# Optimization experiments

Hardware: AMD Instinct MI355X
Metric: run time of the kernel (lower is better)

The kernel has to match this reference:

```python
import jax, jax.numpy as jnp
import numpy as np

B, L, P, D, RD, NT = 128, 128, 1024, 128, 128, 256
SCALE = 1.0 / float(np.sqrt(D))


def _gelu(x):
    return jax.nn.gelu(x, approximate=False)


def _ln(x, g, b):
    mu = jnp.mean(x, axis=-1, keepdims=True)
    v = jnp.mean((x - mu) ** 2, axis=-1, keepdims=True)
    return (x - mu) * jax.lax.rsqrt(v + 1e-5) * g + b


def _mlp2(x, w1, b1, w2, b2):
    return _gelu(x @ w1 + b1) @ w2 + b2


def _l2norm(x):
    return x / jnp.maximum(jnp.sqrt(jnp.sum(x * x, axis=-1, keepdims=True)), 1e-12)


def _params(key):
    ks = jax.random.split(key, 16)
    def lin(k, i, o):
        return jax.random.normal(k, (i, o), jnp.float32) * (1.0 / float(np.sqrt(i)))
    z = lambda *s: jnp.zeros(s, jnp.float32)
    o = lambda *s: jnp.ones(s, jnp.float32)
    p = {}
    p['lt_emb'] = jax.random.normal(ks[0], (NT, D), jnp.float32) * 0.02
    p['lx_w1'] = lin(ks[1], 8, D); p['lx_b1'] = z(D)
    p['lx_w2'] = lin(ks[2], D, D); p['lx_b2'] = z(D)
    p['l_ln_g'] = o(D); p['l_ln_b'] = z(D)
    p['pt_emb'] = jax.random.normal(ks[3], (NT, D), jnp.float32) * 0.02
    p['px_w1'] = lin(ks[4], 192, D); p['px_b1'] = z(D)
    p['px_w2'] = lin(ks[5], D, D); p['px_b2'] = z(D)
    p['ps_w1'] = lin(ks[6], 1, D); p['ps_b1'] = z(D)
    p['ps_w2'] = lin(ks[7], D, D); p['ps_b2'] = z(D)
    p['p_ln_g'] = o(D); p['p_ln_b'] = z(D)
    p['proj_l_w'] = lin(ks[8], D, D)
    p['proj_p_w'] = lin(ks[9], D, D)
    p['dustbin_vec'] = jax.random.normal(ks[10], (D,), jnp.float32) * 0.02
    p['sg_w1'] = lin(ks[11], D, D); p['sg_b1'] = z(D)
    p['sg_w2'] = lin(ks[12], D, 1); p['sg_b2'] = z(1)
    p['retr_l_w'] = lin(ks[13], D, RD)
    p['retr_p_w'] = lin(ks[14], D, RD)
    return p


def setup_inputs():
    key = jax.random.key(0)
    kd = jax.random.split(key, 10)
    inp = {
        'l_x': jax.random.normal(kd[0], (B, L, 8), jnp.float32),
        'l_typ': jax.random.randint(kd[1], (B, L), 0, NT),
        'p_x': jax.random.normal(kd[2], (B, P, 192), jnp.float32),
        'p_typ': jax.random.randint(kd[3], (B, P), 0, NT),
        'p_score': jax.random.normal(kd[4], (B, P), jnp.float32),
        'p_rad': jax.random.uniform(kd[5], (B, P), jnp.float32),
        'l_mask': jax.random.bernoulli(kd[6], 0.9, (B, L)).at[:, 0].set(True),
        'p_mask': jax.random.bernoulli(kd[7], 0.9, (B, P)).at[:, 0].set(True),
    }
    inp.update(_params(kd[8]))
    return inp


def reference(l_x, l_typ, p_x, p_typ, p_score, p_rad, l_mask, p_mask,
              lt_emb, lx_w1, lx_b1, lx_w2, lx_b2, l_ln_g, l_ln_b,
              pt_emb, px_w1, px_b1, px_w2, px_b2, ps_w1, ps_b1, ps_w2, ps_b2,
              p_ln_g, p_ln_b, proj_l_w, proj_p_w, dustbin_vec,
              sg_w1, sg_b1, sg_w2, sg_b2, retr_l_w, retr_p_w):
    # --- encode_batch ---
    hL = _ln(_mlp2(l_x, lx_w1, lx_b1, lx_w2, lx_b2)
             + lt_emb[jnp.clip(l_typ, 0, NT - 1)], l_ln_g, l_ln_b) @ proj_l_w
    hP = _ln(_mlp2(p_x, px_w1, px_b1, px_w2, px_b2)
             + pt_emb[jnp.clip(p_typ, 0, NT - 1)]
             + _mlp2(p_score[..., None], ps_w1, ps_b1, ps_w2, ps_b2), p_ln_g, p_ln_b) @ proj_p_w
    neg = jnp.finfo(jnp.float32).min
    # --- feature_logits_batch: masked bilinear similarity ---
    logits = jnp.einsum('bld,bpd->blp', hL, hP) * SCALE  # [B,L,P]
    logits = jnp.where(p_mask[:, None, :], logits, neg)
    logits = jnp.where(l_mask[:, :, None], logits, neg)
    # --- assignment_logW_batch with dustbin ---
    dust = (hL @ dustbin_vec) * SCALE  # [B,L]
    full = jnp.concatenate([logits, dust[:, :, None]], axis=-1)  # [B,L,P+1]
    full = jnp.where(l_mask[:, :, None], full, neg)
    logW = jax.nn.log_softmax(full, axis=-1)
    # --- invariant_feature_terms_batch ---
    W = jnp.exp(logW)
    lm = l_mask.astype(jnp.float32)
    pm = p_mask.astype(jnp.float32)
    denom = jnp.maximum(lm.sum(axis=1), 1.0)  # [B]
    Wm = jnp.concatenate([W[..., :-1] * pm[:, None, :], W[..., -1:]], axis=-1)
    sharp = (Wm.max(axis=-1) * lm).sum(axis=1) / denom
    ent = ((-(Wm * logW)).sum(axis=-1) * lm).sum(axis=1) / denom
    neg_ent = -ent
    # --- pooled_embeddings_batch ---
    l_g = (hL * lm[..., None]).sum(axis=1) / jnp.maximum(lm.sum(axis=1)[:, None], 1.0)
    p_g = (hP * pm[..., None]).sum(axis=1) / jnp.maximum(pm.sum(axis=1)[:, None], 1.0)
    l_z = _l2norm(l_g @ retr_l_w)
    p_z = _l2norm(p_g @ retr_p_w)
    # --- pocket_sigma_nodes_batch ---
    sig = jax.nn.softplus((_gelu(hP @ sg_w1 + sg_b1) @ sg_w2 + sg_b2)[..., 0]) + 1e-3 + jnp.maximum(p_rad, 0.0)
    return logW, sharp, neg_ent, l_z, p_z, sig
```

## Files before the change

kernel.cpp:

```cpp
#include <hip/hip_runtime.h>
#include <hip/hip_bf16.h>
#include <math.h>

#define B_ 128
#define L_ 128
#define P_ 1024
#define D_ 128
#define NT_ 256

#define NEGF (-__FLT_MAX__)
#define SCALE_ 0.08838834764831845f
#define CLAMPV 1e30f

#define OUT_SHARP  16793600
#define OUT_NEGENT 16793728
#define OUT_LZ     16793856
#define OUT_PZ     16810240
#define OUT_SIG    16826624

#define WS_HLB    0
#define WS_HPB    1048576
#define WS_DUST   9437184
#define WS_SHARPP 9453568
#define WS_ENTP   9454592
#define WS_FLAG   9455616
#define WS_WT     9455632
#define WS_PPART  9500696
#define WS_PCNT   10024984

using bh8  = __attribute__((ext_vector_type(8))) short;
using fx4  = __attribute__((ext_vector_type(4))) float;

__device__ __forceinline__ float gelu_(float x) {
    float c = x * x;
    float v = x * fmaf(c, 0.07135481584f, 1.5957691216f);
    return x * __builtin_amdgcn_rcpf(1.0f + __expf(-v));
}
__device__ __forceinline__ float bf2f(unsigned short u) {
    return __uint_as_float(((unsigned)u) << 16);
}
__device__ __forceinline__ float sanz(float x) {
    return fminf(fmaxf(x, -CLAMPV), CLAMPV);
}
template<int BF> __device__ __forceinline__ float ldf(const void* p, int i) {
    if constexpr (BF) return bf2f(((const unsigned short*)p)[i]);
    else return ((const float*)p)[i];
}
template<int BF> __device__ __forceinline__ void stf(void* p, size_t i, float x) {
    x = sanz(x);
    if constexpr (BF) ((__hip_bfloat16*)p)[i] = __float2bfloat16(x);
    else ((float*)p)[i] = x;
}
__device__ __forceinline__ float maskf(const void* m, int mm, int idx) {
    if (mm == 3) return ((const float*)m)[idx] != 0.f ? 1.f : 0.f;
    if (mm == 2) return ((const unsigned short*)m)[idx] ? 1.f : 0.f;
    if (mm == 1) return ((const unsigned char*)m)[idx] ? 1.f : 0.f;
    return ((const int*)m)[idx] ? 1.f : 0.f;
}
__device__ __forceinline__ int typf(const void* p, int tm, int idx) {
    int v;
    if (tm == 2) v = (int)bf2f(((const unsigned short*)p)[idx]);
    else if (tm == 1) v = (int)((const long long*)p)[idx];
    else v = ((const int*)p)[idx];
    return v < 0 ? 0 : (v > NT_ - 1 ? NT_ - 1 : v);
}

__global__ __launch_bounds__(64) void detect_k(const unsigned int* __restrict__ px,
                                               const unsigned int* __restrict__ pm,
                                               const unsigned int* __restrict__ pt,
                                               int* __restrict__ flags)
{
    const int t = threadIdx.x;
    int hit = 0;
    for (int i = t; i < 4096; i += 64) {
        unsigned e = (px[i] >> 7) & 0xFFu;
        hit += (e >= 110 && e <= 132) ? 1 : 0;
    }
    for (int s = 1; s < 64; s <<= 1) hit += __shfl_xor(hit, s);

    unsigned big = 0, lo3f = 0, hi3f = 0;
    for (int i = t; i < 1024; i += 64) {
        unsigned wv = pm[i];
        big  |= (wv > 1u) ? 1u : 0u;
        lo3f |= ((wv & 0xFFFFu) == 0x3F80u) ? 1u : 0u;
        hi3f |= ((wv >> 16) == 0x3F80u) ? 1u : 0u;
    }
    unsigned long long aBig = __ballot(big != 0), aLo = __ballot(lo3f != 0), aHi = __ballot(hi3f != 0);

    unsigned tbig = 0, oddnz = 0;
    for (int i = t; i < 512; i += 64) {
        unsigned we = pt[2 * i], wo = pt[2 * i + 1];
        tbig  |= (we > 0xFFFFu || wo > 0xFFFFu) ? 1u : 0u;
        oddnz |= (wo != 0u) ? 1u : 0u;
    }
    unsigned long long aTb = __ballot(tbig != 0), aOdd = __ballot(oddnz != 0);

    if (t == 0) {
        flags[1] = (hit > 2048) ? 1 : 0;
        flags[0] = aLo ? 2 : (aHi ? 3 : (aBig ? 1 : 0));
        flags[2] = aTb ? 2 : (!aOdd ? 1 : 0);
    }
}

template<int BF> __device__ __forceinline__ void wt_prep_body(
    const void* w1, const void* w2, const void* sw2,
    const void* proj, const void* gw1, __hip_bfloat16* wt)
{
    const int idx = blockIdx.x * 256 + threadIdx.x;
    const int stride = gridDim.x * 256;
    for (int i = idx; i < 128 * 192; i += stride) {
        int n = i / 192, k = i - n * 192;
        wt[n * 192 + k] = __float2bfloat16(ldf<BF>(w1, k * 128 + n));
    }
    __hip_bfloat16* w2c = wt + 24576;
    for (int i = idx; i < 128 * 256; i += stride) {
        int n = i >> 8, k = i & 255;
        float v = (k < 128) ? ldf<BF>(w2, k * 128 + n) : ldf<BF>(sw2, (k - 128) * 128 + n);
        w2c[n * 256 + k] = __float2bfloat16(v);
    }
    __hip_bfloat16* pjt = wt + 57344;
    for (int i = idx; i < 128 * 128; i += stride) {
        int n = i >> 7, k = i & 127;
        pjt[n * 128 + k] = __float2bfloat16(ldf<BF>(proj, k * 128 + n));
    }
    __hip_bfloat16* g1t = wt + 73728;
    for (int i = idx; i < 128 * 128; i += stride) {
        int n = i >> 7, k = i & 127;
        g1t[n * 128 + k] = __float2bfloat16(ldf<BF>(gw1, k * 128 + n));
    }
}

__global__ __launch_bounds__(256) void wt_prep_k(
    const void* w1, const void* w2, const void* sw2,
    const void* proj, const void* gw1, __hip_bfloat16* wt, const int* flags)
{
    if (flags[1]) wt_prep_body<1>(w1, w2, sw2, proj, gw1, wt);
    else          wt_prep_body<0>(w1, w2, sw2, proj, gw1, wt);
}

#define RL 8
template<int BF> __device__ __forceinline__ void enc_l_body(
    const void* l_x, const void* l_typ, int tm,
    const void* w1, const void* b1, const void* w2, const void* b2,
    const void* lng, const void* lnb, const void* emb, const void* proj,
    const void* dustv, __hip_bfloat16* hLb, float* dust)
{
    __shared__ __align__(16) float X[RL * 8];
    __shared__ __align__(16) float H[RL][D_];
    __shared__ __align__(16) float Y[RL][D_];
    __shared__ float mus[RL], rss[RL];
    const int o = threadIdx.x;
    const int base = blockIdx.x * RL;

    if (o < RL * 8) X[o] = ldf<BF>(l_x, base * 8 + o);
    __syncthreads();

    float acc[RL];
    const float b1o = ldf<BF>(b1, o);
#pragma unroll
    for (int r = 0; r < RL; r++) acc[r] = b1o;
#pragma unroll
    for (int i = 0; i < 8; i += 4) {
        float wa = ldf<BF>(w1, (i + 0) * D_ + o), wb = ldf<BF>(w1, (i + 1) * D_ + o);
        float wc = ldf<BF>(w1, (i + 2) * D_ + o), wd = ldf<BF>(w1, (i + 3) * D_ + o);
#pragma unroll
        for (int r = 0; r < RL; r++) {
            const float4 x4 = *(const float4*)&X[r * 8 + i];
            acc[r] = fmaf(x4.x, wa, fmaf(x4.y, wb, fmaf(x4.z, wc, fmaf(x4.w, wd, acc[r]))));
        }
    }
#pragma unroll
    for (int r = 0; r < RL; r++) H[r][o] = gelu_(acc[r]);
    __syncthreads();

#pragma unroll
    for (int r = 0; r < RL; r++) {
        int tt = typf(l_typ, tm, base + r);
        acc[r] = ldf<BF>(b2, o) + ldf<BF>(emb, tt * D_ + o);
    }
    for (int i = 0; i < D_; i += 4) {
        float wa = ldf<BF>(w2, (i + 0) * D_ + o), wb = ldf<BF>(w2, (i + 1) * D_ + o);
        float wc = ldf<BF>(w2, (i + 2) * D_ + o), wd = ldf<BF>(w2, (i + 3) * D_ + o);
#pragma unroll
        for (int r = 0; r < RL; r++) {
            const float4 h4 = *(const float4*)&H[r][i];
            acc[r] = fmaf(h4.x, wa, fmaf(h4.y, wb, fmaf(h4.z, wc, fmaf(h4.w, wd, acc[r]))));
        }
    }
#pragma unroll
    for (int r = 0; r < RL; r++) Y[r][o] = acc[r];
    __syncthreads();

    {
        const int r = o >> 4, j = o & 15;
        float s = 0.f;
#pragma unroll
        for (int i = 0; i < 8; i++) s += Y[r][j * 8 + i];
        s += __shfl_xor(s, 1); s += __shfl_xor(s, 2); s += __shfl_xor(s, 4); s += __shfl_xor(s, 8);
        const float mu = s * (1.f / 128.f);
        float v = 0.f;
#pragma unroll
        for (int i = 0; i < 8; i++) { float d = Y[r][j * 8 + i] - mu; v = fmaf(d, d, v); }
        v += __shfl_xor(v, 1); v += __shfl_xor(v, 2); v += __shfl_xor(v, 4); v += __shfl_xor(v, 8);
        if (j == 0) { mus[r] = mu; rss[r] = rsqrtf(v * (1.f / 128.f) + 1e-5f); }
    }
    __syncthreads();
    {
        const float g = ldf<BF>(lng, o), bl = ldf<BF>(lnb, o);
#pragma unroll
        for (int r = 0; r < RL; r++) Y[r][o] = fmaf((Y[r][o] - mus[r]) * rss[r], g, bl);
    }
    __syncthreads();

#pragma unroll
    for (int r = 0; r < RL; r++) acc[r] = 0.f;
    for (int i = 0; i < D_; i += 4) {
        float wa = ldf<BF>(proj, (i + 0) * D_ + o), wb = ldf<BF>(proj, (i + 1) * D_ + o);
        float wc = ldf<BF>(proj, (i + 2) * D_ + o), wd = ldf<BF>(proj, (i + 3) * D_ + o);
#pragma unroll
        for (int r = 0; r < RL; r++) {
            const float4 y4 = *(const float4*)&Y[r][i];
            acc[r] = fmaf(y4.x, wa, fmaf(y4.y, wb, fmaf(y4.z, wc, fmaf(y4.w, wd, acc[r]))));
        }
    }
    const float dvo = ldf<BF>(dustv, o);
#pragma unroll
    for (int r = 0; r < RL; r++) {
        hLb[(size_t)(base + r) * D_ + o] = __float2bfloat16(acc[r]);
        H[r][o] = acc[r] * dvo;
    }
    __syncthreads();
    {
        const int r = o >> 4, j = o & 15;
        float s = 0.f;
#pragma unroll
        for (int i = 0; i < 8; i++) s += H[r][j * 8 + i];
        s += __shfl_xor(s, 1); s += __shfl_xor(s, 2); s += __shfl_xor(s, 4); s += __shfl_xor(s, 8);
        if (j == 0) dust[base + r] = s * SCALE_;
    }
}

__global__ __launch_bounds__(128) void enc_l_k(
    const void* l_x, const void* l_typ,
    const void* w1, const void* b1, const void* w2, const void* b2,
    const void* lng, const void* lnb, const void* emb, const void* proj,
    const void* dustv, __hip_bfloat16* hLb, float* dust, const int* flags)
{
    const int tm = flags[2];
    if (flags[1]) enc_l_body<1>(l_x, l_typ, tm, w1, b1, w2, b2, lng, lnb, emb, proj, dustv, hLb, dust);
    else          enc_l_body<0>(l_x, l_typ, tm, w1, b1, w2, b2, lng, lnb, emb, proj, dustv, hLb, dust);
}

#define XS 264
#define ROWS 64
#define ENC_P_SMEM 36608
template<int BF> __device__ __forceinline__ void enc_p_body(
    unsigned short* X, float* red1, float* red2, float* pm_s, float* sc_s, int* tt_s,
    const void* p_x, const void* p_typ, int tm,
    const void* p_score, const void* p_rad,
    const void* b1, const void* b2, const void* sb2,
    const void* sw1, const void* sb1,
    const void* lng, const void* lnb, const void* emb,
    const void* gb1, const void* gw2, const void* gb2,
    const unsigned short* wt, const void* p_mask, int mm,
    void* out, __hip_bfloat16* hPb, float* ppart, float* pcnt)
{
    const int t = threadIdx.x;
    const int o = t & 127, rh = t >> 7;
    const int lane = t & 63, w = t >> 6;
    const int m = lane & 15, g = lane >> 4;
    const int b = blockIdx.x >> 4, tile = blockIdx.x & 15;
    const int base = b * P_ + tile * ROWS;
    const int c0 = 32 * w + m, c1 = 32 * w + 16 + m;
    __hip_bfloat16* Xb = (__hip_bfloat16*)X;

    if constexpr (BF) {
        const unsigned short* src = (const unsigned short*)p_x + (size_t)base * 192;
#pragma unroll
        for (int i = t * 8; i < ROWS * 192; i += 256 * 8) {
            const int r = i / 192, k = i - r * 192;
            *(bh8*)(X + r * XS + k) = *(const bh8*)(src + i);
        }
    } else {
        for (int i = t; i < ROWS * 192; i += 256) {
            int r = i / 192, k = i - r * 192;
            Xb[r * XS + k] = __float2bfloat16(((const float*)p_x)[(size_t)base * 192 + i]);
        }
    }
    if (t < ROWS) {
        pm_s[t] = maskf(p_mask, mm, base + t);
        sc_s[t] = ldf<BF>(p_score, base + t);
        tt_s[t] = typf(p_typ, tm, base + t);
    }
    __syncthreads();

    fx4 A1[4][2];
#pragma unroll
    for (int mt = 0; mt < 4; mt++) { A1[mt][0] = fx4{0,0,0,0}; A1[mt][1] = fx4{0,0,0,0}; }
    {
        const unsigned short* q0 = wt + ((2 * w + 0) * 16 + m) * 192 + g * 8;
        const unsigned short* q1 = wt + ((2 * w + 1) * 16 + m) * 192 + g * 8;
#pragma unroll
        for (int ks = 0; ks < 6; ks++) {
            bh8 f0 = *(const bh8*)(q0 + ks * 32);
            bh8 f1 = *(const bh8*)(q1 + ks * 32);
#pragma unroll
            for (int mt = 0; mt < 4; mt++) {
                bh8 a = *(const bh8*)(X + (mt * 16 + m) * XS + g * 8 + ks * 32);
                A1[mt][0] = __builtin_amdgcn_mfma_f32_16x16x32_bf16(a, f0, A1[mt][0], 0, 0, 0);
                A1[mt][1] = __builtin_amdgcn_mfma_f32_16x16x32_bf16(a, f1, A1[mt][1], 0, 0, 0);
            }
        }
    }
    __syncthreads();

    {
        const float bb0 = ldf<BF>(b1, c0), bb1 = ldf<BF>(b1, c1);
#pragma unroll
        for (int mt = 0; mt < 4; mt++)
#pragma unroll
            for (int j = 0; j < 4; j++) {
                const int row = mt * 16 + g * 4 + j;
                Xb[row * XS + c0] = __float2bfloat16(gelu_(A1[mt][0][j] + bb0));
                Xb[row * XS + c1] = __float2bfloat16(gelu_(A1[mt][1][j] + bb1));
            }
    }
    {
        const float a1v = ldf<BF>(sw1, o), a0v = ldf<BF>(sb1, o);
#pragma unroll
        for (int r = 0; r < 32; r++) {
            const int row = rh * 32 + r;
            Xb[row * XS + 128 + o] = __float2bfloat16(gelu_(fmaf(sc_s[row], a1v, a0v)));
        }
    }
    __syncthreads();

    fx4 A2[4][2];
#pragma unroll
    for (int mt = 0; mt < 4; mt++) { A2[mt][0] = fx4{0,0,0,0}; A2[mt][1] = fx4{0,0,0,0}; }
    {
        const unsigned short* w2cT = wt + 24576;
        const unsigned short* q0 = w2cT + ((2 * w + 0) * 16 + m) * 256 + g * 8;
        const unsigned short* q1 = w2cT + ((2 * w + 1) * 16 + m) * 256 + g * 8;
#pragma unroll
        for (int ks = 0; ks < 8; ks++) {
            bh8 f0 = *(const bh8*)(q0 + ks * 32);
            bh8 f1 = *(const bh8*)(q1 + ks * 32);
#pragma unroll
            for (int mt = 0; mt < 4; mt++) {
                bh8 a = *(const bh8*)(X + (mt * 16 + m) * XS + g * 8 + ks * 32);
                A2[mt][0] = __builtin_amdgcn_mfma_f32_16x16x32_bf16(a, f0, A2[mt][0], 0, 0, 0);
                A2[mt][1] = __builtin_amdgcn_mfma_f32_16x16x32_bf16(a, f1, A2[mt][1], 0, 0, 0);
            }
        }
    }
    {
        const float bc0 = ldf<BF>(b2, c0) + ldf<BF>(sb2, c0);
        const float bc1 = ldf<BF>(b2, c1) + ldf<BF>(sb2, c1);
#pragma unroll
        for (int mt = 0; mt < 4; mt++)
#pragma unroll
            for (int j = 0; j < 4; j++) {
                const int row = mt * 16 + g * 4 + j;
                const int tt = tt_s[row];
                A2[mt][0][j] += bc0 + ldf<BF>(emb, tt * D_ + c0);
                A2[mt][1][j] += bc1 + ldf<BF>(emb, tt * D_ + c1);
            }
    }
#pragma unroll
    for (int mt = 0; mt < 4; mt++)
#pragma unroll
        for (int j = 0; j < 4; j++) {
            const int row = mt * 16 + g * 4 + j;
            float s = A2[mt][0][j] + A2[mt][1][j];
            float q = fmaf(A2[mt][0][j], A2[mt][0][j], A2[mt][1][j] * A2[mt][1][j]);
            s += __shfl_xor(s, 1); s += __shfl_xor(s, 2); s += __shfl_xor(s, 4); s += __shfl_xor(s, 8);
            q += __shfl_xor(q, 1); q += __shfl_xor(q, 2); q += __shfl_xor(q, 4); q += __shfl_xor(q, 8);
            if (m == 0) { red1[row * 4 + w] = s; red2[row * 4 + w] = q; }
        }
    __syncthreads();
    {
        const float gc0 = ldf<BF>(lng, c0), bl0 = ldf<BF>(lnb, c0);
        const float gc1 = ldf<BF>(lng, c1), bl1 = ldf<BF>(lnb, c1);
#pragma unroll
        for (int mt = 0; mt < 4; mt++)
#pragma unroll
            for (int j = 0; j < 4; j++) {
                const int row = mt * 16 + g * 4 + j;
                float S = (red1[row * 4 + 0] + red1[row * 4 + 1]) + (red1[row * 4 + 2] + red1[row * 4 + 3]);
                float Q = (red2[row * 4 + 0] + red2[row * 4 + 1]) + (red2[row * 4 + 2] + red2[row * 4 + 3]);
                float mu = S * (1.f / 128.f);
                float var = fmaf(Q, 1.f / 128.f, -mu * mu);
                float rs = rsqrtf(var + 1e-5f);
                float y0 = fmaf((A2[mt][0][j] - mu) * rs, gc0, bl0);
                float y1 = fmaf((A2[mt][1][j] - mu) * rs, gc1, bl1);
                Xb[row * XS + c0] = __float2bfloat16(y0);
                Xb[row * XS + c1] = __float2bfloat16(y1);
            }
    }
    __syncthreads();

    fx4 A3[4][2];
#pragma unroll
    for (int mt = 0; mt < 4; mt++) { A3[mt][0] = fx4{0,0,0,0}; A3[mt][1] = fx4{0,0,0,0}; }
    {
        const unsigned short* pjT = wt + 57344;
        const unsigned short* q0 = pjT + ((2 * w + 0) * 16 + m) * 128 + g * 8;
        const unsigned short* q1 = pjT + ((2 * w + 1) * 16 + m) * 128 + g * 8;
#pragma unroll
        for (int ks = 0; ks < 4; ks++) {
            bh8 f0 = *(const bh8*)(q0 + ks * 32);
            bh8 f1 = *(const bh8*)(q1 + ks * 32);
#pragma unroll
            for (int mt = 0; mt < 4; mt++) {
                bh8 a = *(const bh8*)(X + (mt * 16 + m) * XS + g * 8 + ks * 32);
                A3[mt][0] = __builtin_amdgcn_mfma_f32_16x16x32_bf16(a, f0, A3[mt][0], 0, 0, 0);
                A3[mt][1] = __builtin_amdgcn_mfma_f32_16x16x32_bf16(a, f1, A3[mt][1], 0, 0, 0);
            }
        }
    }
    __syncthreads();

    {
#pragma unroll
        for (int mt = 0; mt < 4; mt++)
#pragma unroll
            for (int j = 0; j < 4; j++) {
                const int row = mt * 16 + g * 4 + j;
                __hip_bfloat16 h0 = __float2bfloat16(A3[mt][0][j]);
                __hip_bfloat16 h1 = __float2bfloat16(A3[mt][1][j]);
                hPb[(size_t)(base + row) * D_ + c0] = h0;
                hPb[(size_t)(base + row) * D_ + c1] = h1;
                Xb[row * XS + c0] = h0;
                Xb[row * XS + c1] = h1;
            }
        float ps0 = 0.f, ps1 = 0.f;
#pragma unroll
        for (int mt = 0; mt < 4; mt++)
#pragma unroll
            for (int j = 0; j < 4; j++) {
                const int row = mt * 16 + g * 4 + j;
                ps0 = fmaf(A3[mt][0][j], pm_s[row], ps0);
                ps1 = fmaf(A3[mt][1][j], pm_s[row], ps1);
            }
        ps0 += __shfl_xor(ps0, 16); ps0 += __shfl_xor(ps0, 32);
        ps1 += __shfl_xor(ps1, 16); ps1 += __shfl_xor(ps1, 32);
        if (g == 0) {
            ppart[(size_t)blockIdx.x * D_ + c0] = ps0;
            ppart[(size_t)blockIdx.x * D_ + c1] = ps1;
        }
        if (t == 0) {
            float c = 0.f;
#pragma unroll
            for (int r = 0; r < ROWS; r++) c += pm_s[r];
            pcnt[blockIdx.x] = c;
        }
    }
    __syncthreads();

    fx4 A4[4][2];
#pragma unroll
    for (int mt = 0; mt < 4; mt++) { A4[mt][0] = fx4{0,0,0,0}; A4[mt][1] = fx4{0,0,0,0}; }
    {
        const unsigned short* g1T = wt + 73728;
        const unsigned short* q0 = g1T + ((2 * w + 0) * 16 + m) * 128 + g * 8;
        const unsigned short* q1 = g1T + ((2 * w + 1) * 16 + m) * 128 + g * 8;
#pragma unroll
        for (int ks = 0; ks < 4; ks++) {
            bh8 f0 = *(const bh8*)(q0 + ks * 32);
            bh8 f1 = *(const bh8*)(q1 + ks * 32);
#pragma unroll
            for (int mt = 0; mt < 4; mt++) {
                bh8 a = *(const bh8*)(X + (mt * 16 + m) * XS + g * 8 + ks * 32);
                A4[mt][0] = __builtin_amdgcn_mfma_f32_16x16x32_bf16(a, f0, A4[mt][0], 0, 0, 0);
                A4[mt][1] = __builtin_amdgcn_mfma_f32_16x16x32_bf16(a, f1, A4[mt][1], 0, 0, 0);
            }
        }
    }
    {
        const float gb0 = ldf<BF>(gb1, c0), gb1v = ldf<BF>(gb1, c1);
        const float w20 = ldf<BF>(gw2, c0), w21 = ldf<BF>(gw2, c1);
#pragma unroll
        for (int mt = 0; mt < 4; mt++)
#pragma unroll
            for (int j = 0; j < 4; j++) {
                const int row = mt * 16 + g * 4 + j;
                float g0 = gelu_(A4[mt][0][j] + gb0);
                float g1v = gelu_(A4[mt][1][j] + gb1v);
                float p = fmaf(g0, w20, g1v * w21);
                p += __shfl_xor(p, 1); p += __shfl_xor(p, 2); p += __shfl_xor(p, 4); p += __shfl_xor(p, 8);
                if (m == 0) red1[row * 4 + w] = p;
            }
    }
    __syncthreads();
    if (t < ROWS) {
        float s = (red1[t * 4 + 0] + red1[t * 4 + 1]) + (red1[t * 4 + 2] + red1[t * 4 + 3]);
        float v = s + ldf<BF>(gb2, 0);
        float sp = fmaxf(v, 0.f) + log1pf(expf(-fabsf(v)));
        stf<BF>(out, (size_t)OUT_SIG + base + t, sp + 1e-3f + fmaxf(ldf<BF>(p_rad, base + t), 0.f));
    }
}

__global__ __launch_bounds__(256) void enc_p_k(
    const void* p_x, const void* p_typ, const void* p_score, const void* p_rad,
    const void* b1, const void* b2, const void* sb2,
    const void* sw1, const void* sb1,
    const void* lng, const void* lnb, const void* emb,
    const void* gb1, const void* gw2, const void* gb2,
    const unsigned short* wt, const void* p_mask, const int* flags,
    void* out, __hip_bfloat16* hPb, float* ppart, float* pcnt)
{
    extern __shared__ __align__(16) char smem[];
    unsigned short* X = (unsigned short*)smem;
    float* red1 = (float*)(smem + 33792);
    float* red2 = (float*)(smem + 34816);
    float* pm_s = (float*)(smem + 35840);
    float* sc_s = (float*)(smem + 36096);
    int*   tt_s = (int*)(smem + 36352);
    const int tm = flags[2], mm = flags[0];
    if (flags[1]) enc_p_body<1>(X, red1, red2, pm_s, sc_s, tt_s,
                                p_x, p_typ, tm, p_score, p_rad, b1, b2, sb2, sw1, sb1,
                                lng, lnb, emb, gb1, gw2, gb2, wt, p_mask, mm,
                                out, hPb, ppart, pcnt);
    else          enc_p_body<0>(X, red1, red2, pm_s, sc_s, tt_s,
                                p_x, p_typ, tm, p_score, p_rad, b1, b2, sb2, sw1, sb1,
                                lng, lnb, emb, gb1, gw2, gb2, wt, p_mask, mm,
                                out, hPb, ppart, pcnt);
}

template<int BF> __device__ __forceinline__ void logits_sm_body(
    const unsigned short* hLb, const unsigned short* hPb, const float* dust,
    const void* l_mask, const void* p_mask, int mm,
    void* out, float* sharp_parts, float* ent_parts)
{
    __shared__ float pm_s[1024];
    __shared__ float lm_s[16], dv_s[16];
    __shared__ float redA[64], redB[64], redC[64], redD[64], redM[16], redL[16];
    const int t = threadIdx.x;
    const int lane = t & 63, w = t >> 6;
    const int m = lane & 15, g = lane >> 4;
    const int b = blockIdx.x & 127, l0 = (blockIdx.x >> 7) * 16;

    for (int i = t; i < 1024; i += 256) pm_s[i] = maskf(p_mask, mm, b * P_ + i);
    if (t < 16) {
        lm_s[t] = maskf(l_mask, mm, b * L_ + l0 + t);
        dv_s[t] = dust[b * L_ + l0 + t];
    }
    __syncthreads();

    bh8 af[4];
    {
        const unsigned short* ha = hLb + ((size_t)(b * L_ + l0 + m)) * D_ + g * 8;
#pragma unroll
        for (int ks = 0; ks < 4; ks++) af[ks] = *(const bh8*)(ha + ks * 32);
    }
    const unsigned short* hpb = hPb + ((size_t)(b * P_ + w * 256)) * D_;

    fx4 acc[16];
#pragma unroll
    for (int nt = 0; nt < 16; nt++) {
        fx4 c = {0.f, 0.f, 0.f, 0.f};
        const unsigned short* hr = hpb + (nt * 16 + m) * D_ + g * 8;
#pragma unroll
        for (int ks = 0; ks < 4; ks++) {
            bh8 bfr = *(const bh8*)(hr + ks * 32);
            c = __builtin_amdgcn_mfma_f32_16x16x32_bf16(af[ks], bfr, c, 0, 0, 0);
        }
        acc[nt] = c;
    }

    float rmax[4] = {NEGF, NEGF, NEGF, NEGF};
#pragma unroll
    for (int nt = 0; nt < 16; nt++) {
        const float pv = pm_s[w * 256 + nt * 16 + m];
#pragma unroll
        for (int j = 0; j < 4; j++) {
            const bool ok = (lm_s[g * 4 + j] != 0.f) && (pv != 0.f);
            float v = ok ? acc[nt][j] * SCALE_ : NEGF;
            acc[nt][j] = v;
            rmax[j] = fmaxf(rmax[j], v);
        }
    }
#pragma unroll
    for (int j = 0; j < 4; j++) {
        rmax[j] = fmaxf(rmax[j], __shfl_xor(rmax[j], 1));
        rmax[j] = fmaxf(rmax[j], __shfl_xor(rmax[j], 2));
// ... 52 lines not shown
            float lwc = fmaxf(lw, -CLAMPV);
            float wm = __expf(lwc) * pv;
            mw[j] = fmaxf(mw[j], wm);
            if (wm > 0.f) es[j] = fmaf(-wm, lwc, es[j]);
        }
    }
#pragma unroll
    for (int j = 0; j < 4; j++) {
        mw[j] = fmaxf(mw[j], __shfl_xor(mw[j], 1));
        mw[j] = fmaxf(mw[j], __shfl_xor(mw[j], 2));
        mw[j] = fmaxf(mw[j], __shfl_xor(mw[j], 4));
        mw[j] = fmaxf(mw[j], __shfl_xor(mw[j], 8));
        es[j] += __shfl_xor(es[j], 1); es[j] += __shfl_xor(es[j], 2);
        es[j] += __shfl_xor(es[j], 4); es[j] += __shfl_xor(es[j], 8);
    }
    if (m == 0) {
#pragma unroll
        for (int j = 0; j < 4; j++) {
            redC[(g * 4 + j) * 4 + w] = mw[j];
            redD[(g * 4 + j) * 4 + w] = es[j];
        }
    }
    __syncthreads();
    if (t < 16) {
        float dvr = (lm_s[t] != 0.f) ? dv_s[t] : NEGF;
        stf<BF>(out, (size_t)(b * L_ + l0 + t) * (P_ + 1) + P_, dvr - redM[t] - redL[t]);
    }
    if (t == 0) {
        float sp = 0.f, en = 0.f;
        for (int r = 0; r < 16; r++) {
            float dvr = (lm_s[r] != 0.f) ? dv_s[r] : NEGF;
            float lwd = fmaxf(dvr - redM[r] - redL[r], -CLAMPV);
            float wd = __expf(lwd);
            float mwr = fmaxf(fmaxf(redC[r * 4 + 0], redC[r * 4 + 1]), fmaxf(redC[r * 4 + 2], redC[r * 4 + 3]));
            mwr = fmaxf(mwr, wd);
            float esr = (redD[r * 4 + 0] + redD[r * 4 + 1]) + (redD[r * 4 + 2] + redD[r * 4 + 3]);
            if (wd > 0.f) esr = fmaf(-wd, lwd, esr);
            sp = fmaf(mwr, lm_s[r], sp);
            en = fmaf(esr, lm_s[r], en);
        }
        sharp_parts[blockIdx.x] = sp;
        ent_parts[blockIdx.x] = en;
    }
}

__global__ __launch_bounds__(256) void logits_sm_k(
    const unsigned short* hLb, const unsigned short* hPb, const float* dust,
    const void* l_mask, const void* p_mask, const int* flags,
    void* out, float* sharp_parts, float* ent_parts)
{
    const int mm = flags[0];
    if (flags[1]) logits_sm_body<1>(hLb, hPb, dust, l_mask, p_mask, mm, out, sharp_parts, ent_parts);
    else          logits_sm_body<0>(hLb, hPb, dust, l_mask, p_mask, mm, out, sharp_parts, ent_parts);
}

template<int BF> __device__ __forceinline__ void epilogue_body(
    const unsigned short* hLb, const void* l_mask, int mm,
    const void* retr_l, const void* retr_p,
    const float* ppart, const float* pcnt,
    const float* sharp_parts, const float* ent_parts, void* out)
{
    __shared__ float lmv[L_];
    __shared__ __align__(16) float lg[D_];
    __shared__ __align__(16) float pgs[D_];
    __shared__ float red[4];
    const int o = threadIdx.x, b = blockIdx.x;
    lmv[o] = maskf(l_mask, mm, b * L_ + o);
    __syncthreads();
    float cnt = 0.f;
    for (int l = 0; l < L_; l++) cnt += lmv[l];
    {
        float s0 = 0, s1 = 0, s2 = 0, s3 = 0;
        const unsigned short* hb = hLb + (size_t)b * L_ * D_;
        for (int l = 0; l < L_; l += 4) {
            s0 = fmaf(bf2f(hb[(l + 0) * D_ + o]), lmv[l + 0], s0);
            s1 = fmaf(bf2f(hb[(l + 1) * D_ + o]), lmv[l + 1], s1);
            s2 = fmaf(bf2f(hb[(l + 2) * D_ + o]), lmv[l + 2], s2);
            s3 = fmaf(bf2f(hb[(l + 3) * D_ + o]), lmv[l + 3], s3);
        }
        lg[o] = ((s0 + s1) + (s2 + s3)) / fmaxf(cnt, 1.f);
    }
    {
        float s = 0.f, c = 0.f;
        for (int k = 0; k < 16; k++) s += ppart[(size_t)(b * 16 + k) * D_ + o];
        for (int k = 0; k < 16; k++) c += pcnt[b * 16 + k];
        pgs[o] = s / fmaxf(c, 1.f);
    }
    __syncthreads();
    float rL = 0.f, rP = 0.f;
    for (int i = 0; i < D_; i += 4) {
        const float4 g4 = *(const float4*)&lg[i];
        rL = fmaf(g4.x, ldf<BF>(retr_l, (i + 0) * D_ + o), rL);
        rL = fmaf(g4.y, ldf<BF>(retr_l, (i + 1) * D_ + o), rL);
        rL = fmaf(g4.z, ldf<BF>(retr_l, (i + 2) * D_ + o), rL);
        rL = fmaf(g4.w, ldf<BF>(retr_l, (i + 3) * D_ + o), rL);
        const float4 p4 = *(const float4*)&pgs[i];
        rP = fmaf(p4.x, ldf<BF>(retr_p, (i + 0) * D_ + o), rP);
        rP = fmaf(p4.y, ldf<BF>(retr_p, (i + 1) * D_ + o), rP);
        rP = fmaf(p4.z, ldf<BF>(retr_p, (i + 2) * D_ + o), rP);
        rP = fmaf(p4.w, ldf<BF>(retr_p, (i + 3) * D_ + o), rP);
    }
    float nL = rL * rL, nP = rP * rP;
    nL += __shfl_xor(nL, 1); nL += __shfl_xor(nL, 2); nL += __shfl_xor(nL, 4);
    nL += __shfl_xor(nL, 8); nL += __shfl_xor(nL, 16); nL += __shfl_xor(nL, 32);
    nP += __shfl_xor(nP, 1); nP += __shfl_xor(nP, 2); nP += __shfl_xor(nP, 4);
    nP += __shfl_xor(nP, 8); nP += __shfl_xor(nP, 16); nP += __shfl_xor(nP, 32);
    if ((o & 63) == 0) { red[o >> 6] = nL; red[2 + (o >> 6)] = nP; }
    __syncthreads();
    {
        float nrmL = fmaxf(sqrtf(red[0] + red[1]), 1e-12f);
        float nrmP = fmaxf(sqrtf(red[2] + red[3]), 1e-12f);
        stf<BF>(out, (size_t)OUT_LZ + b * D_ + o, rL / nrmL);
        stf<BF>(out, (size_t)OUT_PZ + b * D_ + o, rP / nrmP);
    }
    if (o == 0) {
        const float den = fmaxf(cnt, 1.f);
        float sp = 0.f, en = 0.f;
        for (int k = 0; k < 8; k++) { sp += sharp_parts[k * 128 + b]; en += ent_parts[k * 128 + b]; }
        stf<BF>(out, (size_t)OUT_SHARP + b, sp / den);
        stf<BF>(out, (size_t)OUT_NEGENT + b, -(en / den));
    }
}

__global__ __launch_bounds__(128) void epilogue_k(
    const unsigned short* hLb, const void* l_mask, const int* flags,
    const void* retr_l, const void* retr_p,
    const float* ppart, const float* pcnt,
    const float* sharp_parts, const float* ent_parts, void* out)
{
    const int mm = flags[0];
    if (flags[1]) epilogue_body<1>(hLb, l_mask, mm, retr_l, retr_p, ppart, pcnt, sharp_parts, ent_parts, out);
    else          epilogue_body<0>(hLb, l_mask, mm, retr_l, retr_p, ppart, pcnt, sharp_parts, ent_parts, out);
}

extern "C" void kernel_launch(void* const* d_in, const int* in_sizes, int n_in,
                              void* d_out, int out_size, void* d_ws, size_t ws_size,
                              hipStream_t stream)
{
    const void* l_x     = d_in[0];
    const void* l_typ   = d_in[1];
    const void* p_x     = d_in[2];
    const void* p_typ   = d_in[3];
    const void* p_score = d_in[4];
    const void* p_rad   = d_in[5];
    const void* l_mask  = d_in[6];
    const void* p_mask  = d_in[7];
    const void* lt_emb  = d_in[8];
    const void* lx_w1   = d_in[9];
    const void* lx_b1   = d_in[10];
    const void* lx_w2   = d_in[11];
    const void* lx_b2   = d_in[12];
    const void* l_ln_g  = d_in[13];
    const void* l_ln_b  = d_in[14];
    const void* pt_emb  = d_in[15];
    const void* px_w1   = d_in[16];
    const void* px_b1   = d_in[17];
    const void* px_w2   = d_in[18];
    const void* px_b2   = d_in[19];
    const void* ps_w1   = d_in[20];
    const void* ps_b1   = d_in[21];
    const void* ps_w2   = d_in[22];
    const void* ps_b2   = d_in[23];
    const void* p_ln_g  = d_in[24];
    const void* p_ln_b  = d_in[25];
    const void* proj_l  = d_in[26];
    const void* proj_p  = d_in[27];
    const void* dustv   = d_in[28];
    const void* sg_w1   = d_in[29];
    const void* sg_b1   = d_in[30];
    const void* sg_w2   = d_in[31];
    const void* sg_b2   = d_in[32];
    const void* retr_l  = d_in[33];
    const void* retr_p  = d_in[34];

    float* ws     = (float*)d_ws;
    __hip_bfloat16* hLb = (__hip_bfloat16*)(ws + WS_HLB);
    __hip_bfloat16* hPb = (__hip_bfloat16*)(ws + WS_HPB);
    float* dust   = ws + WS_DUST;
    float* sharpp = ws + WS_SHARPP;
    float* entp   = ws + WS_ENTP;
    int*   flags  = (int*)(ws + WS_FLAG);
    __hip_bfloat16* wt = (__hip_bfloat16*)(ws + WS_WT);
    float* ppart  = ws + WS_PPART;
    float* pcnt   = ws + WS_PCNT;

    detect_k<<<1, 64, 0, stream>>>((const unsigned int*)p_x, (const unsigned int*)p_mask,
                                   (const unsigned int*)p_typ, flags);
    wt_prep_k<<<64, 256, 0, stream>>>(px_w1, px_w2, ps_w2, proj_p, sg_w1, wt, flags);
    enc_l_k<<<(B_ * L_) / RL, 128, 0, stream>>>(l_x, l_typ, lx_w1, lx_b1, lx_w2, lx_b2,
                                                l_ln_g, l_ln_b, lt_emb, proj_l, dustv,
                                                hLb, dust, flags);
    enc_p_k<<<B_ * (P_ / ROWS), 256, ENC_P_SMEM, stream>>>(
        p_x, p_typ, p_score, p_rad,
        px_b1, px_b2, ps_b2, ps_w1, ps_b1,
        p_ln_g, p_ln_b, pt_emb,
        sg_b1, sg_w2, sg_b2,
        (const unsigned short*)wt, p_mask, flags,
        d_out, hPb, ppart, pcnt);
    logits_sm_k<<<B_ * 8, 256, 0, stream>>>((const unsigned short*)hLb, (const unsigned short*)hPb,
                                            dust, l_mask, p_mask, flags, d_out, sharpp, entp);
    epilogue_k<<<B_, 128, 0, stream>>>((const unsigned short*)hLb, l_mask, flags,
                                       retr_l, retr_p, ppart, pcnt, sharpp, entp, d_out);
}
```

Baseline: 204.0 us.

## Precompose proj_p and sg_w1 weights so both GEMMs share one pass

A new small kernel multiplies proj_p by sg_w1 once to form a fused weight, so the sigma head reads the post-LN activations directly instead of hP. This lets the encoder run the projection and the sigma first-layer GEMMs in a single MFMA loop over the same A fragments. It removes two block barriers and the write-back of hP into shared memory. The cost is higher register pressure from doubled accumulators, one extra launch, and slightly different numerics because hP is no longer rounded to bf16 before the second matmul.

```diff
diff --git a/kernel.cpp b/kernel.cpp
--- a/kernel.cpp
+++ b/kernel.cpp
@@ -104,7 +104,7 @@
 
 template<int BF> __device__ __forceinline__ void wt_prep_body(
     const void* w1, const void* w2, const void* sw2,
-    const void* proj, const void* gw1, __hip_bfloat16* wt)
+    const void* proj, __hip_bfloat16* wt)
 {
     const int idx = blockIdx.x * 256 + threadIdx.x;
     const int stride = gridDim.x * 256;
@@ -123,19 +123,39 @@
         int n = i >> 7, k = i & 127;
         pjt[n * 128 + k] = __float2bfloat16(ldf<BF>(proj, k * 128 + n));
     }
-    __hip_bfloat16* g1t = wt + 73728;
-    for (int i = idx; i < 128 * 128; i += stride) {
-        int n = i >> 7, k = i & 127;
-        g1t[n * 128 + k] = __float2bfloat16(ldf<BF>(gw1, k * 128 + n));
-    }
 }
 
 __global__ __launch_bounds__(256) void wt_prep_k(
     const void* w1, const void* w2, const void* sw2,
-    const void* proj, const void* gw1, __hip_bfloat16* wt, const int* flags)
-{
-    if (flags[1]) wt_prep_body<1>(w1, w2, sw2, proj, gw1, wt);
-    else          wt_prep_body<0>(w1, w2, sw2, proj, gw1, wt);
+    const void* proj, __hip_bfloat16* wt, const int* flags)
+{
+    if (flags[1]) wt_prep_body<1>(w1, w2, sw2, proj, wt);
+    else          wt_prep_body<0>(w1, w2, sw2, proj, wt);
+}
+
+__global__ __launch_bounds__(256) void fuse_k(const void* proj, const void* gw1,
+                                              __hip_bfloat16* pg1, const int* flags)
+{
+    const int BF = flags[1];
+    const int tid = blockIdx.x * 256 + threadIdx.x;
+    const int e = tid >> 2, ll = tid & 3;
+    const int n = e >> 7, k = e & 127;
+    float s = 0.f;
+    if (BF) {
+        const unsigned short* pj = (const unsigned short*)proj + k * 128 + ll * 32;
+        const unsigned short* g1 = (const unsigned short*)gw1;
+#pragma unroll 8
+        for (int d = 0; d < 32; d++)
+            s = fmaf(bf2f(pj[d]), bf2f(g1[(ll * 32 + d) * 128 + n]), s);
+    } else {
+        const float* pj = (const float*)proj + k * 128 + ll * 32;
+        const float* g1 = (const float*)gw1;
+#pragma unroll 8
+        for (int d = 0; d < 32; d++)
+            s = fmaf(pj[d], g1[(ll * 32 + d) * 128 + n], s);
+    }
+    s += __shfl_xor(s, 1); s += __shfl_xor(s, 2);
+    if (ll == 0) pg1[n * 128 + k] = __float2bfloat16(s);
 }
 
 #define RL 8
@@ -400,26 +420,35 @@
     }
     __syncthreads();
 
-    fx4 A3[4][2];
-#pragma unroll
-    for (int mt = 0; mt < 4; mt++) { A3[mt][0] = fx4{0,0,0,0}; A3[mt][1] = fx4{0,0,0,0}; }
+    fx4 A3[4][2], A4[4][2];
+#pragma unroll
+    for (int mt = 0; mt < 4; mt++) {
+        A3[mt][0] = fx4{0,0,0,0}; A3[mt][1] = fx4{0,0,0,0};
+        A4[mt][0] = fx4{0,0,0,0}; A4[mt][1] = fx4{0,0,0,0};
+    }
     {
         const unsigned short* pjT = wt + 57344;
-        const unsigned short* q0 = pjT + ((2 * w + 0) * 16 + m) * 128 + g * 8;
-        const unsigned short* q1 = pjT + ((2 * w + 1) * 16 + m) * 128 + g * 8;
+        const unsigned short* pg1 = wt + 73728;
+        const unsigned short* q30 = pjT + ((2 * w + 0) * 16 + m) * 128 + g * 8;
+        const unsigned short* q31 = pjT + ((2 * w + 1) * 16 + m) * 128 + g * 8;
+        const unsigned short* q40 = pg1 + ((2 * w + 0) * 16 + m) * 128 + g * 8;
+        const unsigned short* q41 = pg1 + ((2 * w + 1) * 16 + m) * 128 + g * 8;
 #pragma unroll
         for (int ks = 0; ks < 4; ks++) {
-            bh8 f0 = *(const bh8*)(q0 + ks * 32);
-            bh8 f1 = *(const bh8*)(q1 + ks * 32);
+            bh8 f30 = *(const bh8*)(q30 + ks * 32);
+            bh8 f31 = *(const bh8*)(q31 + ks * 32);
+            bh8 f40 = *(const bh8*)(q40 + ks * 32);
+            bh8 f41 = *(const bh8*)(q41 + ks * 32);
 #pragma unroll
             for (int mt = 0; mt < 4; mt++) {
                 bh8 a = *(const bh8*)(X + (mt * 16 + m) * XS + g * 8 + ks * 32);
-                A3[mt][0] = __builtin_amdgcn_mfma_f32_16x16x32_bf16(a, f0, A3[mt][0], 0, 0, 0);
-                A3[mt][1] = __builtin_amdgcn_mfma_f32_16x16x32_bf16(a, f1, A3[mt][1], 0, 0, 0);
+                A3[mt][0] = __builtin_amdgcn_mfma_f32_16x16x32_bf16(a, f30, A3[mt][0], 0, 0, 0);
+                A3[mt][1] = __builtin_amdgcn_mfma_f32_16x16x32_bf16(a, f31, A3[mt][1], 0, 0, 0);
+                A4[mt][0] = __builtin_amdgcn_mfma_f32_16x16x32_bf16(a, f40, A4[mt][0], 0, 0, 0);
+                A4[mt][1] = __builtin_amdgcn_mfma_f32_16x16x32_bf16(a, f41, A4[mt][1], 0, 0, 0);
             }
         }
     }
-    __syncthreads();
 
     {
 #pragma unroll
@@ -427,12 +456,8 @@
 #pragma unroll
             for (int j = 0; j < 4; j++) {
                 const int row = mt * 16 + g * 4 + j;
-                __hip_bfloat16 h0 = __float2bfloat16(A3[mt][0][j]);
-                __hip_bfloat16 h1 = __float2bfloat16(A3[mt][1][j]);
-                hPb[(size_t)(base + row) * D_ + c0] = h0;
-                hPb[(size_t)(base + row) * D_ + c1] = h1;
-                Xb[row * XS + c0] = h0;
-                Xb[row * XS + c1] = h1;
+                hPb[(size_t)(base + row) * D_ + c0] = __float2bfloat16(A3[mt][0][j]);
+                hPb[(size_t)(base + row) * D_ + c1] = __float2bfloat16(A3[mt][1][j]);
             }
         float ps0 = 0.f, ps1 = 0.f;
 #pragma unroll
@@ -456,27 +481,7 @@
             pcnt[blockIdx.x] = c;
         }
     }
-    __syncthreads();
-
-    fx4 A4[4][2];
-#pragma unroll
-    for (int mt = 0; mt < 4; mt++) { A4[mt][0] = fx4{0,0,0,0}; A4[mt][1] = fx4{0,0,0,0}; }
-    {
-        const unsigned short* g1T = wt + 73728;
-        const unsigned short* q0 = g1T + ((2 * w + 0) * 16 + m) * 128 + g * 8;
-        const unsigned short* q1 = g1T + ((2 * w + 1) * 16 + m) * 128 + g * 8;
-#pragma unroll
-        for (int ks = 0; ks < 4; ks++) {
-            bh8 f0 = *(const bh8*)(q0 + ks * 32);
-            bh8 f1 = *(const bh8*)(q1 + ks * 32);
-#pragma unroll
-            for (int mt = 0; mt < 4; mt++) {
-                bh8 a = *(const bh8*)(X + (mt * 16 + m) * XS + g * 8 + ks * 32);
-                A4[mt][0] = __builtin_amdgcn_mfma_f32_16x16x32_bf16(a, f0, A4[mt][0], 0, 0, 0);
-                A4[mt][1] = __builtin_amdgcn_mfma_f32_16x16x32_bf16(a, f1, A4[mt][1], 0, 0, 0);
-            }
-        }
-    }
+
     {
         const float gb0 = ldf<BF>(gb1, c0), gb1v = ldf<BF>(gb1, c1);
         const float w20 = ldf<BF>(gw2, c0), w21 = ldf<BF>(gw2, c1);
@@ -824,7 +829,8 @@
 
     detect_k<<<1, 64, 0, stream>>>((const unsigned int*)p_x, (const unsigned int*)p_mask,
                                    (const unsigned int*)p_typ, flags);
-    wt_prep_k<<<64, 256, 0, stream>>>(px_w1, px_w2, ps_w2, proj_p, sg_w1, wt, flags);
+    wt_prep_k<<<64, 256, 0, stream>>>(px_w1, px_w2, ps_w2, proj_p, wt, flags);
+    fuse_k<<<256, 256, 0, stream>>>(proj_p, sg_w1, wt + 73728, flags);
     enc_l_k<<<(B_ * L_) / RL, 128, 0, stream>>>(l_x, l_typ, lx_w1, lx_b1, lx_w2, lx_b2,
                                                 l_ln_g, l_ln_b, lt_emb, proj_l, dustv,
                                                 hLb, dust, flags);
```

New measurement: 220.0 us. +7.9%, slower.

## Split pocket encoder tile across 8 waves with 2x4 M/N wave grid

Applied to the files above, without the earlier changes.

The pocket encoder block grows from 256 to 512 threads. Waves are arranged as 2 row groups by 4 column groups, so each wave computes 32 rows instead of 64 in every MFMA stage. Per-thread accumulator registers are halved and each block gets more waves to hide LDS and MFMA latency. In exchange, each wave group writes its own pooled partial sum, so the epilogue reduces 32 partials per batch, and the ppart workspace must hold twice as many entries.

```diff
diff --git a/kernel.cpp b/kernel.cpp
--- a/kernel.cpp
+++ b/kernel.cpp
@@ -268,21 +268,23 @@
     const int t = threadIdx.x;
     const int o = t & 127, rh = t >> 7;
     const int lane = t & 63, w = t >> 6;
+    const int wn = w & 3, wm = w >> 2;
     const int m = lane & 15, g = lane >> 4;
     const int b = blockIdx.x >> 4, tile = blockIdx.x & 15;
     const int base = b * P_ + tile * ROWS;
-    const int c0 = 32 * w + m, c1 = 32 * w + 16 + m;
+    const int c0 = 32 * wn + m, c1 = 32 * wn + 16 + m;
+    const int mtb = 2 * wm;
     __hip_bfloat16* Xb = (__hip_bfloat16*)X;
 
     if constexpr (BF) {
         const unsigned short* src = (const unsigned short*)p_x + (size_t)base * 192;
 #pragma unroll
-        for (int i = t * 8; i < ROWS * 192; i += 256 * 8) {
+        for (int i = t * 8; i < ROWS * 192; i += 512 * 8) {
             const int r = i / 192, k = i - r * 192;
             *(bh8*)(X + r * XS + k) = *(const bh8*)(src + i);
         }
     } else {
-        for (int i = t; i < ROWS * 192; i += 256) {
+        for (int i = t; i < ROWS * 192; i += 512) {
             int r = i / 192, k = i - r * 192;
             Xb[r * XS + k] = __float2bfloat16(((const float*)p_x)[(size_t)base * 192 + i]);
         }
@@ -294,19 +296,19 @@
     }
     __syncthreads();
 
-    fx4 A1[4][2];
-#pragma unroll
-    for (int mt = 0; mt < 4; mt++) { A1[mt][0] = fx4{0,0,0,0}; A1[mt][1] = fx4{0,0,0,0}; }
-    {
-        const unsigned short* q0 = wt + ((2 * w + 0) * 16 + m) * 192 + g * 8;
-        const unsigned short* q1 = wt + ((2 * w + 1) * 16 + m) * 192 + g * 8;
+    fx4 A1[2][2];
+#pragma unroll
+    for (int mt = 0; mt < 2; mt++) { A1[mt][0] = fx4{0,0,0,0}; A1[mt][1] = fx4{0,0,0,0}; }
+    {
+        const unsigned short* q0 = wt + ((2 * wn + 0) * 16 + m) * 192 + g * 8;
+        const unsigned short* q1 = wt + ((2 * wn + 1) * 16 + m) * 192 + g * 8;
 #pragma unroll
         for (int ks = 0; ks < 6; ks++) {
             bh8 f0 = *(const bh8*)(q0 + ks * 32);
             bh8 f1 = *(const bh8*)(q1 + ks * 32);
 #pragma unroll
-            for (int mt = 0; mt < 4; mt++) {
-                bh8 a = *(const bh8*)(X + (mt * 16 + m) * XS + g * 8 + ks * 32);
+            for (int mt = 0; mt < 2; mt++) {
+                bh8 a = *(const bh8*)(X + ((mtb + mt) * 16 + m) * XS + g * 8 + ks * 32);
                 A1[mt][0] = __builtin_amdgcn_mfma_f32_16x16x32_bf16(a, f0, A1[mt][0], 0, 0, 0);
                 A1[mt][1] = __builtin_amdgcn_mfma_f32_16x16x32_bf16(a, f1, A1[mt][1], 0, 0, 0);
             }
@@ -317,10 +319,10 @@
     {
         const float bb0 = ldf<BF>(b1, c0), bb1 = ldf<BF>(b1, c1);
 #pragma unroll
-        for (int mt = 0; mt < 4; mt++)
+        for (int mt = 0; mt < 2; mt++)
 #pragma unroll
             for (int j = 0; j < 4; j++) {
-                const int row = mt * 16 + g * 4 + j;
+                const int row = (mtb + mt) * 16 + g * 4 + j;
                 Xb[row * XS + c0] = __float2bfloat16(gelu_(A1[mt][0][j] + bb0));
                 Xb[row * XS + c1] = __float2bfloat16(gelu_(A1[mt][1][j] + bb1));
             }
@@ -328,27 +330,27 @@
     {
         const float a1v = ldf<BF>(sw1, o), a0v = ldf<BF>(sb1, o);
 #pragma unroll
-        for (int r = 0; r < 32; r++) {
-            const int row = rh * 32 + r;
+        for (int r = 0; r < 16; r++) {
+            const int row = rh * 16 + r;
             Xb[row * XS + 128 + o] = __float2bfloat16(gelu_(fmaf(sc_s[row], a1v, a0v)));
         }
     }
     __syncthreads();
 
-    fx4 A2[4][2];
-#pragma unroll
-    for (int mt = 0; mt < 4; mt++) { A2[mt][0] = fx4{0,0,0,0}; A2[mt][1] = fx4{0,0,0,0}; }
+    fx4 A2[2][2];
+#pragma unroll
+    for (int mt = 0; mt < 2; mt++) { A2[mt][0] = fx4{0,0,0,0}; A2[mt][1] = fx4{0,0,0,0}; }
     {
         const unsigned short* w2cT = wt + 24576;
-        const unsigned short* q0 = w2cT + ((2 * w + 0) * 16 + m) * 256 + g * 8;
-        const unsigned short* q1 = w2cT + ((2 * w + 1) * 16 + m) * 256 + g * 8;
+        const unsigned short* q0 = w2cT + ((2 * wn + 0) * 16 + m) * 256 + g * 8;
+        const unsigned short* q1 = w2cT + ((2 * wn + 1) * 16 + m) * 256 + g * 8;
 #pragma unroll
         for (int ks = 0; ks < 8; ks++) {
             bh8 f0 = *(const bh8*)(q0 + ks * 32);
             bh8 f1 = *(const bh8*)(q1 + ks * 32);
 #pragma unroll
-            for (int mt = 0; mt < 4; mt++) {
-                bh8 a = *(const bh8*)(X + (mt * 16 + m) * XS + g * 8 + ks * 32);
+            for (int mt = 0; mt < 2; mt++) {
+                bh8 a = *(const bh8*)(X + ((mtb + mt) * 16 + m) * XS + g * 8 + ks * 32);
                 A2[mt][0] = __builtin_amdgcn_mfma_f32_16x16x32_bf16(a, f0, A2[mt][0], 0, 0, 0);
                 A2[mt][1] = __builtin_amdgcn_mfma_f32_16x16x32_bf16(a, f1, A2[mt][1], 0, 0, 0);
             }
@@ -358,35 +360,35 @@
         const float bc0 = ldf<BF>(b2, c0) + ldf<BF>(sb2, c0);
         const float bc1 = ldf<BF>(b2, c1) + ldf<BF>(sb2, c1);
 #pragma unroll
-        for (int mt = 0; mt < 4; mt++)
+        for (int mt = 0; mt < 2; mt++)
 #pragma unroll
             for (int j = 0; j < 4; j++) {
-                const int row = mt * 16 + g * 4 + j;
+                const int row = (mtb + mt) * 16 + g * 4 + j;
                 const int tt = tt_s[row];
                 A2[mt][0][j] += bc0 + ldf<BF>(emb, tt * D_ + c0);
                 A2[mt][1][j] += bc1 + ldf<BF>(emb, tt * D_ + c1);
             }
     }
 #pragma unroll
-    for (int mt = 0; mt < 4; mt++)
+    for (int mt = 0; mt < 2; mt++)
 #pragma unroll
         for (int j = 0; j < 4; j++) {
-            const int row = mt * 16 + g * 4 + j;
+            const int row = (mtb + mt) * 16 + g * 4 + j;
             float s = A2[mt][0][j] + A2[mt][1][j];
             float q = fmaf(A2[mt][0][j], A2[mt][0][j], A2[mt][1][j] * A2[mt][1][j]);
             s += __shfl_xor(s, 1); s += __shfl_xor(s, 2); s += __shfl_xor(s, 4); s += __shfl_xor(s, 8);
             q += __shfl_xor(q, 1); q += __shfl_xor(q, 2); q += __shfl_xor(q, 4); q += __shfl_xor(q, 8);
-            if (m == 0) { red1[row * 4 + w] = s; red2[row * 4 + w] = q; }
+            if (m == 0) { red1[row * 4 + wn] = s; red2[row * 4 + wn] = q; }
         }
     __syncthreads();
     {
         const float gc0 = ldf<BF>(lng, c0), bl0 = ldf<BF>(lnb, c0);
         const float gc1 = ldf<BF>(lng, c1), bl1 = ldf<BF>(lnb, c1);
 #pragma unroll
-        for (int mt = 0; mt < 4; mt++)
+        for (int mt = 0; mt < 2; mt++)
 #pragma unroll
             for (int j = 0; j < 4; j++) {
-                const int row = mt * 16 + g * 4 + j;
+                const int row = (mtb + mt) * 16 + g * 4 + j;
                 float S = (red1[row * 4 + 0] + red1[row * 4 + 1]) + (red1[row * 4 + 2] + red1[row * 4 + 3]);
                 float Q = (red2[row * 4 + 0] + red2[row * 4 + 1]) + (red2[row * 4 + 2] + red2[row * 4 + 3]);
                 float mu = S * (1.f / 128.f);
@@ -400,20 +402,20 @@
     }
     __syncthreads();
 
-    fx4 A3[4][2];
-#pragma unroll
-    for (int mt = 0; mt < 4; mt++) { A3[mt][0] = fx4{0,0,0,0}; A3[mt][1] = fx4{0,0,0,0}; }
+    fx4 A3[2][2];
+#pragma unroll
+    for (int mt = 0; mt < 2; mt++) { A3[mt][0] = fx4{0,0,0,0}; A3[mt][1] = fx4{0,0,0,0}; }
     {
         const unsigned short* pjT = wt + 57344;
-        const unsigned short* q0 = pjT + ((2 * w + 0) * 16 + m) * 128 + g * 8;
-        const unsigned short* q1 = pjT + ((2 * w + 1) * 16 + m) * 128 + g * 8;
+        const unsigned short* q0 = pjT + ((2 * wn + 0) * 16 + m) * 128 + g * 8;
+        const unsigned short* q1 = pjT + ((2 * wn + 1) * 16 + m) * 128 + g * 8;
 #pragma unroll
         for (int ks = 0; ks < 4; ks++) {
             bh8 f0 = *(const bh8*)(q0 + ks * 32);
             bh8 f1 = *(const bh8*)(q1 + ks * 32);
 #pragma unroll
-            for (int mt = 0; mt < 4; mt++) {
-                bh8 a = *(const bh8*)(X + (mt * 16 + m) * XS + g * 8 + ks * 32);
+            for (int mt = 0; mt < 2; mt++) {
+                bh8 a = *(const bh8*)(X + ((mtb + mt) * 16 + m) * XS + g * 8 + ks * 32);
                 A3[mt][0] = __builtin_amdgcn_mfma_f32_16x16x32_bf16(a, f0, A3[mt][0], 0, 0, 0);
                 A3[mt][1] = __builtin_amdgcn_mfma_f32_16x16x32_bf16(a, f1, A3[mt][1], 0, 0, 0);
             }
@@ -423,10 +425,10 @@
 
     {
 #pragma unroll
-        for (int mt = 0; mt < 4; mt++)
+        for (int mt = 0; mt < 2; mt++)
 #pragma unroll
             for (int j = 0; j < 4; j++) {
-                const int row = mt * 16 + g * 4 + j;
+                const int row = (mtb + mt) * 16 + g * 4 + j;
                 __hip_bfloat16 h0 = __float2bfloat16(A3[mt][0][j]);
                 __hip_bfloat16 h1 = __float2bfloat16(A3[mt][1][j]);
                 hPb[(size_t)(base + row) * D_ + c0] = h0;
@@ -436,18 +438,18 @@
             }
         float ps0 = 0.f, ps1 = 0.f;
 #pragma unroll
-        for (int mt = 0; mt < 4; mt++)
+        for (int mt = 0; mt < 2; mt++)
 #pragma unroll
             for (int j = 0; j < 4; j++) {
-                const int row = mt * 16 + g * 4 + j;
+                const int row = (mtb + mt) * 16 + g * 4 + j;
                 ps0 = fmaf(A3[mt][0][j], pm_s[row], ps0);
                 ps1 = fmaf(A3[mt][1][j], pm_s[row], ps1);
             }
         ps0 += __shfl_xor(ps0, 16); ps0 += __shfl_xor(ps0, 32);
         ps1 += __shfl_xor(ps1, 16); ps1 += __shfl_xor(ps1, 32);
         if (g == 0) {
-            ppart[(size_t)blockIdx.x * D_ + c0] = ps0;
-            ppart[(size_t)blockIdx.x * D_ + c1] = ps1;
+            ppart[(size_t)(blockIdx.x * 2 + wm) * D_ + c0] = ps0;
+            ppart[(size_t)(blockIdx.x * 2 + wm) * D_ + c1] = ps1;
         }
         if (t == 0) {
             float c = 0.f;
@@ -458,20 +460,20 @@
     }
     __syncthreads();
 
-    fx4 A4[4][2];
-#pragma unroll
-    for (int mt = 0; mt < 4; mt++) { A4[mt][0] = fx4{0,0,0,0}; A4[mt][1] = fx4{0,0,0,0}; }
+    fx4 A4[2][2];
+#pragma unroll
+    for (int mt = 0; mt < 2; mt++) { A4[mt][0] = fx4{0,0,0,0}; A4[mt][1] = fx4{0,0,0,0}; }
     {
         const unsigned short* g1T = wt + 73728;
-        const unsigned short* q0 = g1T + ((2 * w + 0) * 16 + m) * 128 + g * 8;
-        const unsigned short* q1 = g1T + ((2 * w + 1) * 16 + m) * 128 + g * 8;
+        const unsigned short* q0 = g1T + ((2 * wn + 0) * 16 + m) * 128 + g * 8;
+        const unsigned short* q1 = g1T + ((2 * wn + 1) * 16 + m) * 128 + g * 8;
 #pragma unroll
         for (int ks = 0; ks < 4; ks++) {
             bh8 f0 = *(const bh8*)(q0 + ks * 32);
             bh8 f1 = *(const bh8*)(q1 + ks * 32);
 #pragma unroll
-            for (int mt = 0; mt < 4; mt++) {
-                bh8 a = *(const bh8*)(X + (mt * 16 + m) * XS + g * 8 + ks * 32);
+            for (int mt = 0; mt < 2; mt++) {
+                bh8 a = *(const bh8*)(X + ((mtb + mt) * 16 + m) * XS + g * 8 + ks * 32);
                 A4[mt][0] = __builtin_amdgcn_mfma_f32_16x16x32_bf16(a, f0, A4[mt][0], 0, 0, 0);
                 A4[mt][1] = __builtin_amdgcn_mfma_f32_16x16x32_bf16(a, f1, A4[mt][1], 0, 0, 0);
             }
@@ -481,15 +483,15 @@
         const float gb0 = ldf<BF>(gb1, c0), gb1v = ldf<BF>(gb1, c1);
         const float w20 = ldf<BF>(gw2, c0), w21 = ldf<BF>(gw2, c1);
 #pragma unroll
-        for (int mt = 0; mt < 4; mt++)
+        for (int mt = 0; mt < 2; mt++)
 #pragma unroll
             for (int j = 0; j < 4; j++) {
-                const int row = mt * 16 + g * 4 + j;
+                const int row = (mtb + mt) * 16 + g * 4 + j;
                 float g0 = gelu_(A4[mt][0][j] + gb0);
                 float g1v = gelu_(A4[mt][1][j] + gb1v);
                 float p = fmaf(g0, w20, g1v * w21);
                 p += __shfl_xor(p, 1); p += __shfl_xor(p, 2); p += __shfl_xor(p, 4); p += __shfl_xor(p, 8);
-                if (m == 0) red1[row * 4 + w] = p;
+                if (m == 0) red1[row * 4 + wn] = p;
             }
     }
     __syncthreads();
@@ -501,7 +503,7 @@
     }
 }
 
-__global__ __launch_bounds__(256) void enc_p_k(
+__global__ __launch_bounds__(512) void enc_p_k(
     const void* p_x, const void* p_typ, const void* p_score, const void* p_rad,
     const void* b1, const void* b2, const void* sb2,
     const void* sw1, const void* sb1,
@@ -720,7 +722,7 @@
     }
     {
         float s = 0.f, c = 0.f;
-        for (int k = 0; k < 16; k++) s += ppart[(size_t)(b * 16 + k) * D_ + o];
+        for (int k = 0; k < 32; k++) s += ppart[(size_t)(b * 32 + k) * D_ + o];
         for (int k = 0; k < 16; k++) c += pcnt[b * 16 + k];
         pgs[o] = s / fmaxf(c, 1.f);
     }
@@ -828,7 +830,7 @@
     enc_l_k<<<(B_ * L_) / RL, 128, 0, stream>>>(l_x, l_typ, lx_w1, lx_b1, lx_w2, lx_b2,
                                                 l_ln_g, l_ln_b, lt_emb, proj_l, dustv,
                                                 hLb, dust, flags);
-    enc_p_k<<<B_ * (P_ / ROWS), 256, ENC_P_SMEM, stream>>>(
+    enc_p_k<<<B_ * (P_ / ROWS), 512, ENC_P_SMEM, stream>>>(
         p_x, p_typ, p_score, p_rad,
         px_b1, px_b2, ps_b2, ps_w1, ps_b1,
         p_ln_g, p_ln_b, pt_emb,
```

New measurement: 230.9 us. +13.2%, slower.
